# Kernel tuning notes

Measured on AMD Instinct MI355X. Metric: run time of the kernel, lower is better.

## Reference

```python
import jax, jax.numpy as jnp
import numpy as np

NUM_EXPERTS = 8
TOP_K = 2
N_EMBD = 1024
BLOCKING = 128
D_FFN = ((4 * N_EMBD // TOP_K) + BLOCKING - 1) // BLOCKING * BLOCKING  # 2048


def setup_inputs() -> dict:
    key = jax.random.key(0)
    k_x, k_r, k_w1, k_w2 = jax.random.split(key, 4)
    B, S = 4, 2048
    x = jax.random.normal(k_x, (B, S, N_EMBD), dtype=jnp.float32)
    # nn.Linear weight layout: [out_features, in_features]
    router_w = jax.random.normal(k_r, (NUM_EXPERTS, N_EMBD), dtype=jnp.float32) * 0.02
    # trunc_normal(std=0.02, a=-0.06, b=0.06) approximated by clipped normal
    w1 = jnp.clip(jax.random.normal(k_w1, (N_EMBD, NUM_EXPERTS * D_FFN), dtype=jnp.float32) * 0.02, -0.06, 0.06)
    w2 = jnp.clip(jax.random.normal(k_w2, (NUM_EXPERTS * D_FFN, N_EMBD), dtype=jnp.float32) * 0.02, -0.06, 0.06)
    return {"x": x, "router_w": router_w, "w1": w1, "w2": w2}


def reference(x, router_w, w1, w2):
    B, S, D = x.shape
    T = B * S
    x_flat = x.reshape(T, D)

    # Router
    router_logits = x_flat @ router_w.T                       # [T, E]
    router_probs = jax.nn.softmax(router_logits.astype(jnp.float32), axis=-1)
    expert_weights, selected_experts = jax.lax.top_k(router_probs, TOP_K)  # [T, K]
    expert_weights = expert_weights / expert_weights.sum(axis=-1, keepdims=True)
    expert_weights = expert_weights.astype(x.dtype)

    # Combine weights c[t, e] = sum_k weight[t, k] * [sel[t, k] == e]
    combine = jnp.zeros((T, NUM_EXPERTS), dtype=x.dtype)
    combine = combine.at[jnp.arange(T)[:, None], selected_experts].add(expert_weights)

    # Expert FFNs (math equivalent of block-sparse sdd/gelu/dsd + scatter-combine)
    w1r = w1.reshape(D, NUM_EXPERTS, D_FFN)
    w2r = w2.reshape(NUM_EXPERTS, D_FFN, D)
    out_flat = jnp.zeros((T, D), dtype=x.dtype)
    for e in range(NUM_EXPERTS):
        h = jax.nn.gelu(x_flat @ w1r[:, e, :], approximate=False)  # [T, d_ffn]
        out_flat = out_flat + combine[:, e:e + 1] * (h @ w2r[e])
    output = out_flat.reshape(B, S, D)

    # Aux losses
    router_z_loss = jnp.mean(jax.nn.logsumexp(router_logits, axis=-1) ** 2)
    p_i = router_probs.mean(axis=0)                           # [E]
    f_i = jnp.zeros((NUM_EXPERTS,), dtype=x.dtype).at[selected_experts.reshape(-1)].add(
        jnp.float32(1.0) / (T * TOP_K))
    load_balance_loss = NUM_EXPERTS * jnp.dot(f_i, p_i.astype(x.dtype))

    return output, router_z_loss, load_balance_loss, f_i
```

## Files before the change

kernel.cpp:

```cpp
#include <hip/hip_runtime.h>
#include <hip/hip_bf16.h>
#include <math.h>

#define T_TOK   8192
#define D_MODEL 1024
#define DFFN    2048
#define N_EXP   8
#define NASSIGN (T_TOK*2)

#define BM 128
#define BN 128
#define BK 32
#define BKP 40
#define TILE_MAX 144

#define WS_ZSUM     0
#define WS_PSUM     4
#define WS_COUNTS   64
#define WS_CURSOR   96
#define WS_OFFS     128
#define WS_NTILES   160
#define WS_TMAP     256
#define WS_SEL      4096
#define WS_WGT      69632
#define WS_AIDX     135168
#define WS_AW       200704
#define WS_H        266240

typedef __attribute__((ext_vector_type(8))) short bf16x8;
typedef __attribute__((ext_vector_type(4))) float f32x4;
typedef __attribute__((ext_vector_type(4))) unsigned int u32x4;

static __device__ __forceinline__ unsigned short f2bf(float f) {
    unsigned int u = __builtin_bit_cast(unsigned int, f);
    u += 0x7fffu + ((u >> 16) & 1u);
    return (unsigned short)(u >> 16);
}

__global__ __launch_bounds__(256) void router_kernel(
    const float* __restrict__ x, const float* __restrict__ rw,
    float* zsum, float* psum, int* counts, int* sel, float* wgt)
{
    __shared__ float xs[32*129];
    __shared__ float rs[8*129];
    __shared__ float lg[32*9];
    __shared__ float blk_p[8];
    __shared__ int   blk_c[8];
    __shared__ float blk_z;
    int tid = threadIdx.x;
    if (tid < 8) { blk_p[tid] = 0.f; blk_c[tid] = 0; }
    if (tid == 8) blk_z = 0.f;
    int tb = blockIdx.x * 32;
    int tt = tid >> 3, e = tid & 7;
    float acc = 0.f;
    for (int c = 0; c < 8; ++c) {
        int c0 = c * 128;
        #pragma unroll
        for (int p = 0; p < 16; ++p) {
            int flat = p * 256 + tid;
            int r = flat >> 7, col = flat & 127;
            xs[r*129 + col] = x[(size_t)(tb + r)*D_MODEL + c0 + col];
        }
        #pragma unroll
        for (int p = 0; p < 4; ++p) {
            int flat = p * 256 + tid;
            int er = flat >> 7, col = flat & 127;
            rs[er*129 + col] = rw[(size_t)er*D_MODEL + c0 + col];
        }
        __syncthreads();
        #pragma unroll 8
        for (int i = 0; i < 128; ++i)
            acc += xs[tt*129 + i] * rs[e*129 + i];
        __syncthreads();
    }
    lg[tt*9 + e] = acc;
    __syncthreads();
    if (tid < 32) {
        int t = tb + tid;
        float l[8], p[8];
        float mx = -1e30f;
        #pragma unroll
        for (int j = 0; j < 8; ++j) { l[j] = lg[tid*9 + j]; mx = fmaxf(mx, l[j]); }
        float se = 0.f;
        #pragma unroll
        for (int j = 0; j < 8; ++j) { p[j] = expf(l[j] - mx); se += p[j]; }
        float inv = 1.f / se;
        #pragma unroll
        for (int j = 0; j < 8; ++j) p[j] *= inv;
        float lse = mx + logf(se);
        atomicAdd(&blk_z, lse*lse);
        #pragma unroll
        for (int j = 0; j < 8; ++j) atomicAdd(&blk_p[j], p[j]);
        int i0 = 0; float b0 = p[0];
        #pragma unroll
        for (int j = 1; j < 8; ++j) if (p[j] > b0) { b0 = p[j]; i0 = j; }
        int i1 = -1; float b1 = -1.f;
        #pragma unroll
        for (int j = 0; j < 8; ++j) if (j != i0 && p[j] > b1) { b1 = p[j]; i1 = j; }
        float s = b0 + b1;
        sel[t*2+0] = i0; sel[t*2+1] = i1;
        wgt[t*2+0] = b0 / s; wgt[t*2+1] = b1 / s;
        atomicAdd(&blk_c[i0], 1); atomicAdd(&blk_c[i1], 1);
    }
    __syncthreads();
    if (tid < 8) {
        atomicAdd(&counts[tid], blk_c[tid]);
        unsafeAtomicAdd(&psum[tid], blk_p[tid]);
    }
    if (tid == 8) unsafeAtomicAdd(zsum, blk_z);
}

__global__ void finalize_kernel(const int* counts, const float* psum, const float* zsum,
                                int* offs, int* ntiles, int* tmap, float* out_tail)
{
    if (threadIdx.x != 0) return;
    int off = 0, nt = 0;
    float lb = 0.f;
    for (int e = 0; e < N_EXP; ++e) {
        int c = counts[e];
        offs[e] = off;
        for (int m0 = 0; m0 < c; m0 += BM) {
            tmap[nt*4+0] = e;
            tmap[nt*4+1] = off + m0;
            tmap[nt*4+2] = min(BM, c - m0);
            tmap[nt*4+3] = 0;
            nt++;
        }
        float fi = (float)c / (float)NASSIGN;
        out_tail[2 + e] = fi;
        lb += fi * (psum[e] / (float)T_TOK);
        off += c;
    }
    *ntiles = nt;
    out_tail[0] = zsum[0] / (float)T_TOK;
    out_tail[1] = (float)N_EXP * lb;
}

__global__ __launch_bounds__(256) void scatter_kernel(
    const int* __restrict__ sel, const float* __restrict__ wgt,
    const int* __restrict__ offs, int* cursor, int* aidx, float* aw)
{
    int t = blockIdx.x * 256 + threadIdx.x;
    if (t >= T_TOK) return;
    #pragma unroll
    for (int k = 0; k < 2; ++k) {
        int e = sel[t*2 + k];
        int pos = atomicAdd(&cursor[e], 1);
        int r = offs[e] + pos;
        aidx[r] = t;
        aw[r] = wgt[t*2 + k];
    }
}

__global__ __launch_bounds__(256) void gemm1_kernel(
    const float* __restrict__ x, const float* __restrict__ w1,
    const int* __restrict__ aidx, const int* __restrict__ tmap,
    const int* __restrict__ ntiles, unsigned short* __restrict__ H)
{
    int tile = blockIdx.y;
    if (tile >= *ntiles) return;
    int e     = tmap[tile*4+0];
    int gr    = tmap[tile*4+1];
    int valid = tmap[tile*4+2];
    int n0 = blockIdx.x * BN;
    __shared__ unsigned short As[BM*BKP];
    __shared__ unsigned short Bs[BN*BKP];
    int tid = threadIdx.x;
    int lane = tid & 63, wave = tid >> 6;
    int wm = (wave & 1) * 64, wn = (wave >> 1) * 64;
    int q = lane >> 4, r16 = lane & 15;
    f32x4 acc[4][4];
    #pragma unroll
    for (int i = 0; i < 4; ++i) {
        #pragma unroll
        for (int j = 0; j < 4; ++j) acc[i][j] = (f32x4){0.f, 0.f, 0.f, 0.f};
    }
    int arow = tid >> 3;
    int ac4  = (tid & 7) * 4;
    int rowtok[4];
    #pragma unroll
    for (int p = 0; p < 4; ++p) {
        int m = arow + p*32;
        rowtok[p] = aidx[gr + min(m, valid - 1)];
    }
    int bn  = tid & 127;
    int bkq = (tid >> 7) * 16;
    const size_t bcol = (size_t)e * DFFN + n0 + bn;

    for (int kt = 0; kt < D_MODEL / BK; ++kt) {
        int k0 = kt * BK;
        #pragma unroll
        for (int p = 0; p < 4; ++p) {
            int m = arow + p*32;
            const float4 v = *(const float4*)(x + (size_t)rowtok[p]*D_MODEL + k0 + ac4);
            ushort4 h;
            h.x = f2bf(v.x); h.y = f2bf(v.y); h.z = f2bf(v.z); h.w = f2bf(v.w);
            *(ushort4*)&As[m*BKP + ac4] = h;
        }
        #pragma unroll
        for (int p = 0; p < 4; ++p) {
            int kb = bkq + p*4;
            float v0 = w1[(size_t)(k0 + kb + 0)*(N_EXP*DFFN) + bcol];
            float v1 = w1[(size_t)(k0 + kb + 1)*(N_EXP*DFFN) + bcol];
            float v2 = w1[(size_t)(k0 + kb + 2)*(N_EXP*DFFN) + bcol];
            float v3 = w1[(size_t)(k0 + kb + 3)*(N_EXP*DFFN) + bcol];
            ushort4 h;
            h.x = f2bf(v0); h.y = f2bf(v1); h.z = f2bf(v2); h.w = f2bf(v3);
            *(ushort4*)&Bs[bn*BKP + kb] = h;
        }
        __syncthreads();
        bf16x8 af[4], bfr[4];
        #pragma unroll
        for (int im = 0; im < 4; ++im)
            af[im] = *(const bf16x8*)&As[(wm + im*16 + r16)*BKP + q*8];
        #pragma unroll
        for (int in = 0; in < 4; ++in)
            bfr[in] = *(const bf16x8*)&Bs[(wn + in*16 + r16)*BKP + q*8];
        #pragma unroll
        for (int im = 0; im < 4; ++im) {
            #pragma unroll
            for (int in = 0; in < 4; ++in)
                acc[im][in] = __builtin_amdgcn_mfma_f32_16x16x32_bf16(af[im], bfr[in], acc[im][in], 0, 0, 0);
        }
        __syncthreads();
    }
    #pragma unroll
    for (int im = 0; im < 4; ++im) {
        #pragma unroll
        for (int reg = 0; reg < 4; ++reg) {
            int m = wm + im*16 + q*4 + reg;
            if (m < valid) {
                size_t rowbase = (size_t)(gr + m) * DFFN + n0 + wn;
                #pragma unroll
                for (int in = 0; in < 4; ++in) {
                    float v = acc[im][in][reg];
                    float g = 0.5f * v * (1.0f + erff(v * 0.70710678118654752f));
                    H[rowbase + in*16 + r16] = f2bf(g);
                }
            }
        }
    }
}

__global__ __launch_bounds__(256) void gemm2_kernel(
    const unsigned short* __restrict__ H, const float* __restrict__ w2,
    const int* __restrict__ aidx, const float* __restrict__ aw,
    const int* __restrict__ tmap, const int* __restrict__ ntiles,
    float* __restrict__ out)
{
    int tile = blockIdx.y;
    if (tile >= *ntiles) return;
    int e     = tmap[tile*4+0];
    int gr    = tmap[tile*4+1];
    int valid = tmap[tile*4+2];
    int n0 = blockIdx.x * BN;
    __shared__ unsigned short As[BM*BKP];
    __shared__ unsigned short Bs[BN*BKP];
    int tid = threadIdx.x;
    int lane = tid & 63, wave = tid >> 6;
    int wm = (wave & 1) * 64, wn = (wave >> 1) * 64;
    int q = lane >> 4, r16 = lane & 15;
    f32x4 acc[4][4];
    #pragma unroll
    for (int i = 0; i < 4; ++i) {
        #pragma unroll
        for (int j = 0; j < 4; ++j) acc[i][j] = (f32x4){0.f, 0.f, 0.f, 0.f};
    }
    int am = tid >> 1, ah = (tid & 1) * 16;
    int amr = min(am, valid - 1);
    const unsigned short* hrow = H + (size_t)(gr + amr)*DFFN + ah;
    int bn  = tid & 127;
    int bkq = (tid >> 7) * 16;
    const size_t bcol = n0 + bn;

    for (int kt = 0; kt < DFFN / BK; ++kt) {
        int k0 = kt * BK;
        {
            const u32x4 v0 = *(const u32x4*)(hrow + k0);
            const u32x4 v1 = *(const u32x4*)(hrow + k0 + 8);
            *(u32x4*)&As[am*BKP + ah]     = v0;
            *(u32x4*)&As[am*BKP + ah + 8] = v1;
        }
        #pragma unroll
        for (int p = 0; p < 4; ++p) {
            int kb = bkq + p*4;
            float v0 = w2[(size_t)(e*DFFN + k0 + kb + 0)*D_MODEL + bcol];
            float v1 = w2[(size_t)(e*DFFN + k0 + kb + 1)*D_MODEL + bcol];
            float v2 = w2[(size_t)(e*DFFN + k0 + kb + 2)*D_MODEL + bcol];
            float v3 = w2[(size_t)(e*DFFN + k0 + kb + 3)*D_MODEL + bcol];
            ushort4 h;
            h.x = f2bf(v0); h.y = f2bf(v1); h.z = f2bf(v2); h.w = f2bf(v3);
            *(ushort4*)&Bs[bn*BKP + kb] = h;
        }
        __syncthreads();
        bf16x8 af[4], bfr[4];
        #pragma unroll
        for (int im = 0; im < 4; ++im)
            af[im] = *(const bf16x8*)&As[(wm + im*16 + r16)*BKP + q*8];
        #pragma unroll
        for (int in = 0; in < 4; ++in)
            bfr[in] = *(const bf16x8*)&Bs[(wn + in*16 + r16)*BKP + q*8];
        #pragma unroll
        for (int im = 0; im < 4; ++im) {
            #pragma unroll
            for (int in = 0; in < 4; ++in)
                acc[im][in] = __builtin_amdgcn_mfma_f32_16x16x32_bf16(af[im], bfr[in], acc[im][in], 0, 0, 0);
        }
        __syncthreads();
    }
    #pragma unroll
    for (int im = 0; im < 4; ++im) {
        #pragma unroll
        for (int reg = 0; reg < 4; ++reg) {
            int m = wm + im*16 + q*4 + reg;
            if (m < valid) {
                int t = aidx[gr + m];
                float w = aw[gr + m];
                float* orow = out + (size_t)t*D_MODEL + n0 + wn;
                #pragma unroll
                for (int in = 0; in < 4; ++in)
                    unsafeAtomicAdd(&orow[in*16 + r16], w * acc[im][in][reg]);
            }
        }
    }
}

extern "C" void kernel_launch(void* const* d_in, const int* in_sizes, int n_in,
                              void* d_out, int out_size, void* d_ws, size_t ws_size,
                              hipStream_t stream)
{
    const float* x  = (const float*)d_in[0];
    const float* rw = (const float*)d_in[1];
    const float* w1 = (const float*)d_in[2];
    const float* w2 = (const float*)d_in[3];
    float* out = (float*)d_out;
    char* ws = (char*)d_ws;
    float* zsum   = (float*)(ws + WS_ZSUM);
    float* psum   = (float*)(ws + WS_PSUM);
    int*   counts = (int*)(ws + WS_COUNTS);
    int*   cursor = (int*)(ws + WS_CURSOR);
    int*   offs   = (int*)(ws + WS_OFFS);
    int*   ntiles = (int*)(ws + WS_NTILES);
    int*   tmap   = (int*)(ws + WS_TMAP);
    int*   sel    = (int*)(ws + WS_SEL);
    float* wgt    = (float*)(ws + WS_WGT);
    int*   aidx   = (int*)(ws + WS_AIDX);
    float* aw     = (float*)(ws + WS_AW);
    unsigned short* H = (unsigned short*)(ws + WS_H);

    hipMemsetAsync(d_out, 0, (size_t)T_TOK * D_MODEL * sizeof(float), stream);
    hipMemsetAsync(ws, 0, 256, stream);

    router_kernel<<<T_TOK/32, 256, 0, stream>>>(x, rw, zsum, psum, counts, sel, wgt);
    finalize_kernel<<<1, 64, 0, stream>>>(counts, psum, zsum, offs, ntiles, tmap,
                                          out + (size_t)T_TOK * D_MODEL);
    scatter_kernel<<<T_TOK/256, 256, 0, stream>>>(sel, wgt, offs, cursor, aidx, aw);
    gemm1_kernel<<<dim3(DFFN/BN, TILE_MAX), 256, 0, stream>>>(x, w1, aidx, tmap, ntiles, H);
    gemm2_kernel<<<dim3(D_MODEL/BN, TILE_MAX), 256, 0, stream>>>(H, w2, aidx, aw, tmap, ntiles, out);
}
```

Baseline: 713.1 us.

## Pre-convert x and weights to bf16 K-major and stream tiles via global_load_lds

Adds prepass kernels that convert x to bf16 and transpose-convert w1/w2 to bf16 with K contiguous, so the GEMM kernels can load tiles with 16-byte global_load_lds directly into unpadded LDS. This removes the per-tile fp32 loads, strided column gathers and in-loop bf16 conversions from both GEMMs. The trade-offs are an extra pass over about 100 MB of fp32 input per call, a larger workspace, and possible LDS bank conflicts now that the row padding is gone.

```diff
diff --git a/kernel.cpp b/kernel.cpp
--- a/kernel.cpp
+++ b/kernel.cpp
@@ -11,7 +11,6 @@
 #define BM 128
 #define BN 128
 #define BK 32
-#define BKP 40
 #define TILE_MAX 144
 
 #define WS_ZSUM     0
@@ -25,7 +24,10 @@
 #define WS_WGT      69632
 #define WS_AIDX     135168
 #define WS_AW       200704
-#define WS_H        266240
+#define WS_XB       266240
+#define WS_W1T      (WS_XB + 16777216)
+#define WS_W2T      (WS_W1T + 33554432)
+#define WS_H        (WS_W2T + 33554432)
 
 typedef __attribute__((ext_vector_type(8))) short bf16x8;
 typedef __attribute__((ext_vector_type(4))) float f32x4;
@@ -35,6 +37,53 @@
     unsigned int u = __builtin_bit_cast(unsigned int, f);
     u += 0x7fffu + ((u >> 16) & 1u);
     return (unsigned short)(u >> 16);
+}
+
+static __device__ __forceinline__ void gll16(const unsigned short* g, unsigned short* l) {
+    __builtin_amdgcn_global_load_lds(
+        (const __attribute__((address_space(1))) unsigned int*)g,
+        (__attribute__((address_space(3))) unsigned int*)l, 16, 0, 0);
+}
+
+__global__ __launch_bounds__(256) void cvt_x_kernel(const float* __restrict__ in,
+                                                    unsigned short* __restrict__ out)
+{
+    int i = (blockIdx.x * 256 + threadIdx.x) * 8;
+    float4 a = *(const float4*)(in + i);
+    float4 b = *(const float4*)(in + i + 4);
+    unsigned short t[8];
+    t[0]=f2bf(a.x); t[1]=f2bf(a.y); t[2]=f2bf(a.z); t[3]=f2bf(a.w);
+    t[4]=f2bf(b.x); t[5]=f2bf(b.y); t[6]=f2bf(b.z); t[7]=f2bf(b.w);
+    *(u32x4*)(out + i) = *(u32x4*)t;
+}
+
+__global__ __launch_bounds__(256) void transpose_cvt_kernel(
+    const float* __restrict__ in, unsigned short* __restrict__ out, int K, int N)
+{
+    int e = blockIdx.z;
+    const float* inp = in + (size_t)e * K * N;
+    unsigned short* outp = out + (size_t)e * K * N;
+    __shared__ unsigned short tile[64][68];
+    int k0 = blockIdx.y * 64, n0 = blockIdx.x * 64;
+    int tid = threadIdx.x;
+    int r = tid >> 4, c4 = (tid & 15) * 4;
+    #pragma unroll
+    for (int p = 0; p < 4; ++p) {
+        int k = r + p * 16;
+        float4 v = *(const float4*)(inp + (size_t)(k0 + k) * N + n0 + c4);
+        tile[k][c4+0] = f2bf(v.x);
+        tile[k][c4+1] = f2bf(v.y);
+        tile[k][c4+2] = f2bf(v.z);
+        tile[k][c4+3] = f2bf(v.w);
+    }
+    __syncthreads();
+    int n = tid >> 2, kc = (tid & 3) * 16;
+    unsigned short t[16];
+    #pragma unroll
+    for (int j = 0; j < 16; ++j) t[j] = tile[kc + j][n];
+    unsigned short* o = outp + (size_t)(n0 + n) * K + k0 + kc;
+    *(u32x4*)o       = *(u32x4*)t;
+    *(u32x4*)(o + 8) = *(u32x4*)(t + 8);
 }
 
 __global__ __launch_bounds__(256) void router_kernel(
@@ -153,7 +202,7 @@
 }
 
 __global__ __launch_bounds__(256) void gemm1_kernel(
-    const float* __restrict__ x, const float* __restrict__ w1,
+    const unsigned short* __restrict__ xb, const unsigned short* __restrict__ w1t,
     const int* __restrict__ aidx, const int* __restrict__ tmap,
     const int* __restrict__ ntiles, unsigned short* __restrict__ H)
 {
@@ -163,65 +212,51 @@
     int gr    = tmap[tile*4+1];
     int valid = tmap[tile*4+2];
     int n0 = blockIdx.x * BN;
-    __shared__ unsigned short As[BM*BKP];
-    __shared__ unsigned short Bs[BN*BKP];
+    __shared__ unsigned short As[BM*BK];
+    __shared__ unsigned short Bs[BN*BK];
     int tid = threadIdx.x;
     int lane = tid & 63, wave = tid >> 6;
     int wm = (wave & 1) * 64, wn = (wave >> 1) * 64;
     int q = lane >> 4, r16 = lane & 15;
     f32x4 acc[4][4];
     #pragma unroll
-    for (int i = 0; i < 4; ++i) {
+    for (int i = 0; i < 4; ++i)
         #pragma unroll
         for (int j = 0; j < 4; ++j) acc[i][j] = (f32x4){0.f, 0.f, 0.f, 0.f};
-    }
-    int arow = tid >> 3;
-    int ac4  = (tid & 7) * 4;
-    int rowtok[4];
-    #pragma unroll
-    for (int p = 0; p < 4; ++p) {
-        int m = arow + p*32;
-        rowtok[p] = aidx[gr + min(m, valid - 1)];
-    }
-    int bn  = tid & 127;
-    int bkq = (tid >> 7) * 16;
-    const size_t bcol = (size_t)e * DFFN + n0 + bn;
+
+    int c0 = tid, c1 = 256 + tid;
+    int m0c = c0 >> 2, k0c = (c0 & 3) * 8;
+    int m1c = c1 >> 2, k1c = (c1 & 3) * 8;
+    int tok0 = aidx[gr + min(m0c, valid - 1)];
+    int tok1 = aidx[gr + min(m1c, valid - 1)];
+    const unsigned short* ga0 = xb + (size_t)tok0 * D_MODEL + k0c;
+    const unsigned short* ga1 = xb + (size_t)tok1 * D_MODEL + k1c;
+    const unsigned short* gb0 = w1t + ((size_t)(e * DFFN + n0 + m0c)) * D_MODEL + k0c;
+    const unsigned short* gb1 = w1t + ((size_t)(e * DFFN + n0 + m1c)) * D_MODEL + k1c;
+    unsigned short* lA0 = As + c0 * 8;
+    unsigned short* lA1 = As + c1 * 8;
+    unsigned short* lB0 = Bs + c0 * 8;
+    unsigned short* lB1 = Bs + c1 * 8;
 
     for (int kt = 0; kt < D_MODEL / BK; ++kt) {
-        int k0 = kt * BK;
-        #pragma unroll
-        for (int p = 0; p < 4; ++p) {
-            int m = arow + p*32;
-            const float4 v = *(const float4*)(x + (size_t)rowtok[p]*D_MODEL + k0 + ac4);
-            ushort4 h;
-            h.x = f2bf(v.x); h.y = f2bf(v.y); h.z = f2bf(v.z); h.w = f2bf(v.w);
-            *(ushort4*)&As[m*BKP + ac4] = h;
-        }
-        #pragma unroll
-        for (int p = 0; p < 4; ++p) {
-            int kb = bkq + p*4;
-            float v0 = w1[(size_t)(k0 + kb + 0)*(N_EXP*DFFN) + bcol];
-            float v1 = w1[(size_t)(k0 + kb + 1)*(N_EXP*DFFN) + bcol];
-            float v2 = w1[(size_t)(k0 + kb + 2)*(N_EXP*DFFN) + bcol];
-            float v3 = w1[(size_t)(k0 + kb + 3)*(N_EXP*DFFN) + bcol];
-            ushort4 h;
-            h.x = f2bf(v0); h.y = f2bf(v1); h.z = f2bf(v2); h.w = f2bf(v3);
-            *(ushort4*)&Bs[bn*BKP + kb] = h;
-        }
+        int kofs = kt * BK;
+        gll16(ga0 + kofs, lA0);
+        gll16(ga1 + kofs, lA1);
+        gll16(gb0 + kofs, lB0);
+        gll16(gb1 + kofs, lB1);
         __syncthreads();
         bf16x8 af[4], bfr[4];
         #pragma unroll
         for (int im = 0; im < 4; ++im)
-            af[im] = *(const bf16x8*)&As[(wm + im*16 + r16)*BKP + q*8];
+            af[im] = *(const bf16x8*)&As[(wm + im*16 + r16)*BK + q*8];
         #pragma unroll
         for (int in = 0; in < 4; ++in)
-            bfr[in] = *(const bf16x8*)&Bs[(wn + in*16 + r16)*BKP + q*8];
-        #pragma unroll
-        for (int im = 0; im < 4; ++im) {
+            bfr[in] = *(const bf16x8*)&Bs[(wn + in*16 + r16)*BK + q*8];
+        #pragma unroll
+        for (int im = 0; im < 4; ++im)
             #pragma unroll
             for (int in = 0; in < 4; ++in)
                 acc[im][in] = __builtin_amdgcn_mfma_f32_16x16x32_bf16(af[im], bfr[in], acc[im][in], 0, 0, 0);
-        }
         __syncthreads();
     }
     #pragma unroll
@@ -243,7 +278,7 @@
 }
 
 __global__ __launch_bounds__(256) void gemm2_kernel(
-    const unsigned short* __restrict__ H, const float* __restrict__ w2,
+    const unsigned short* __restrict__ H, const unsigned short* __restrict__ w2t,
     const int* __restrict__ aidx, const float* __restrict__ aw,
     const int* __restrict__ tmap, const int* __restrict__ ntiles,
     float* __restrict__ out)
@@ -254,58 +289,49 @@
     int gr    = tmap[tile*4+1];
     int valid = tmap[tile*4+2];
     int n0 = blockIdx.x * BN;
-    __shared__ unsigned short As[BM*BKP];
-    __shared__ unsigned short Bs[BN*BKP];
+    __shared__ unsigned short As[BM*BK];
+    __shared__ unsigned short Bs[BN*BK];
     int tid = threadIdx.x;
     int lane = tid & 63, wave = tid >> 6;
     int wm = (wave & 1) * 64, wn = (wave >> 1) * 64;
     int q = lane >> 4, r16 = lane & 15;
     f32x4 acc[4][4];
     #pragma unroll
-    for (int i = 0; i < 4; ++i) {
+    for (int i = 0; i < 4; ++i)
         #pragma unroll
         for (int j = 0; j < 4; ++j) acc[i][j] = (f32x4){0.f, 0.f, 0.f, 0.f};
-    }
-    int am = tid >> 1, ah = (tid & 1) * 16;
-    int amr = min(am, valid - 1);
-    const unsigned short* hrow = H + (size_t)(gr + amr)*DFFN + ah;
-    int bn  = tid & 127;
-    int bkq = (tid >> 7) * 16;
-    const size_t bcol = n0 + bn;
+
+    int c0 = tid, c1 = 256 + tid;
+    int m0c = c0 >> 2, k0c = (c0 & 3) * 8;
+    int m1c = c1 >> 2, k1c = (c1 & 3) * 8;
+    const unsigned short* ga0 = H + (size_t)(gr + min(m0c, valid - 1)) * DFFN + k0c;
+    const unsigned short* ga1 = H + (size_t)(gr + min(m1c, valid - 1)) * DFFN + k1c;
+    const unsigned short* gb0 = w2t + (size_t)e * (DFFN * D_MODEL) + (size_t)(n0 + m0c) * DFFN + k0c;
+    const unsigned short* gb1 = w2t + (size_t)e * (DFFN * D_MODEL) + (size_t)(n0 + m1c) * DFFN + k1c;
+    unsigned short* lA0 = As + c0 * 8;
+    unsigned short* lA1 = As + c1 * 8;
+    unsigned short* lB0 = Bs + c0 * 8;
+    unsigned short* lB1 = Bs + c1 * 8;
 
     for (int kt = 0; kt < DFFN / BK; ++kt) {
-        int k0 = kt * BK;
-        {
-            const u32x4 v0 = *(const u32x4*)(hrow + k0);
-            const u32x4 v1 = *(const u32x4*)(hrow + k0 + 8);
-            *(u32x4*)&As[am*BKP + ah]     = v0;
-            *(u32x4*)&As[am*BKP + ah + 8] = v1;
-        }
-        #pragma unroll
-        for (int p = 0; p < 4; ++p) {
-            int kb = bkq + p*4;
-            float v0 = w2[(size_t)(e*DFFN + k0 + kb + 0)*D_MODEL + bcol];
-            float v1 = w2[(size_t)(e*DFFN + k0 + kb + 1)*D_MODEL + bcol];
-            float v2 = w2[(size_t)(e*DFFN + k0 + kb + 2)*D_MODEL + bcol];
-            float v3 = w2[(size_t)(e*DFFN + k0 + kb + 3)*D_MODEL + bcol];
-            ushort4 h;
-            h.x = f2bf(v0); h.y = f2bf(v1); h.z = f2bf(v2); h.w = f2bf(v3);
-            *(ushort4*)&Bs[bn*BKP + kb] = h;
-        }
+        int kofs = kt * BK;
+        gll16(ga0 + kofs, lA0);
+        gll16(ga1 + kofs, lA1);
+        gll16(gb0 + kofs, lB0);
+        gll16(gb1 + kofs, lB1);
         __syncthreads();
         bf16x8 af[4], bfr[4];
         #pragma unroll
         for (int im = 0; im < 4; ++im)
-            af[im] = *(const bf16x8*)&As[(wm + im*16 + r16)*BKP + q*8];
+            af[im] = *(const bf16x8*)&As[(wm + im*16 + r16)*BK + q*8];
         #pragma unroll
         for (int in = 0; in < 4; ++in)
-            bfr[in] = *(const bf16x8*)&Bs[(wn + in*16 + r16)*BKP + q*8];
-        #pragma unroll
-        for (int im = 0; im < 4; ++im) {
+            bfr[in] = *(const bf16x8*)&Bs[(wn + in*16 + r16)*BK + q*8];
+        #pragma unroll
+        for (int im = 0; im < 4; ++im)
             #pragma unroll
             for (int in = 0; in < 4; ++in)
                 acc[im][in] = __builtin_amdgcn_mfma_f32_16x16x32_bf16(af[im], bfr[in], acc[im][in], 0, 0, 0);
-        }
         __syncthreads();
     }
     #pragma unroll
@@ -346,15 +372,22 @@
     float* wgt    = (float*)(ws + WS_WGT);
     int*   aidx   = (int*)(ws + WS_AIDX);
     float* aw     = (float*)(ws + WS_AW);
-    unsigned short* H = (unsigned short*)(ws + WS_H);
+    unsigned short* xb  = (unsigned short*)(ws + WS_XB);
+    unsigned short* w1t = (unsigned short*)(ws + WS_W1T);
+    unsigned short* w2t = (unsigned short*)(ws + WS_W2T);
+    unsigned short* H   = (unsigned short*)(ws + WS_H);
 
     hipMemsetAsync(d_out, 0, (size_t)T_TOK * D_MODEL * sizeof(float), stream);
     hipMemsetAsync(ws, 0, 256, stream);
+
+    cvt_x_kernel<<<T_TOK*D_MODEL/(256*8), 256, 0, stream>>>(x, xb);
+    transpose_cvt_kernel<<<dim3(16384/64, 1024/64, 1), 256, 0, stream>>>(w1, w1t, 1024, 16384);
+    transpose_cvt_kernel<<<dim3(1024/64, 2048/64, 8), 256, 0, stream>>>(w2, w2t, 2048, 1024);
 
     router_kernel<<<T_TOK/32, 256, 0, stream>>>(x, rw, zsum, psum, counts, sel, wgt);
     finalize_kernel<<<1, 64, 0, stream>>>(counts, psum, zsum, offs, ntiles, tmap,
                                           out + (size_t)T_TOK * D_MODEL);
     scatter_kernel<<<T_TOK/256, 256, 0, stream>>>(sel, wgt, offs, cursor, aidx, aw);
-    gemm1_kernel<<<dim3(DFFN/BN, TILE_MAX), 256, 0, stream>>>(x, w1, aidx, tmap, ntiles, H);
-    gemm2_kernel<<<dim3(D_MODEL/BN, TILE_MAX), 256, 0, stream>>>(H, w2, aidx, aw, tmap, ntiles, out);
-}
+    gemm1_kernel<<<dim3(DFFN/BN, TILE_MAX), 256, 0, stream>>>(xb, w1t, aidx, tmap, ntiles, H);
+    gemm2_kernel<<<dim3(D_MODEL/BN, TILE_MAX), 256, 0, stream>>>(H, w2t, aidx, aw, tmap, ntiles, out);
+}
```

Result: faster. 613.2 us (-14.0%).
